# Performance work log

Measured on AMD Instinct MI355X. Metric: run time of the kernel, lower is better.

The kernel has to match this reference:

```python
import jax, jax.numpy as jnp
import numpy as np

NEG_INF = -9e15
ALPHA = 0.2  # leaky relu negative slope


def setup_inputs() -> dict:
    key = jax.random.key(0)
    ks = jax.random.split(key, 7)
    B, N, FIN, FOUT = 4, 2048, 512, 128
    inp = {
        "input": jax.random.normal(ks[0], (B, N, FIN), dtype=jnp.float32),
        "W": jax.random.normal(ks[1], (FIN, FOUT), dtype=jnp.float32) * (1.414 / np.sqrt(FIN)),
        "a1": jax.random.normal(ks[2], (FOUT, 1), dtype=jnp.float32) * 0.1,
        "a2": jax.random.normal(ks[3], (FOUT, 1), dtype=jnp.float32) * 0.1,
        "adj": jax.random.randint(ks[4], (B, N, N), 0, 4, dtype=jnp.int32),
        "adj_tree": jax.random.randint(ks[5], (B, N, N), 0, 4, dtype=jnp.int32),
        "d1": 1,
        "d2": 2,
    }
    return inp


def reference(input, W, a1, a2, adj, adj_tree, d1, d2):
    # adj_tree is accepted but unused by the original forward.
    h = jnp.einsum("bnf,fo->bno", input, W)          # [B,N,out]
    t1 = jnp.einsum("bno,ok->bnk", h, a1)            # [B,N,1]
    t2 = jnp.einsum("bno,ok->bnk", h, a2)            # [B,N,1]
    # e[b,i,j] = t1[b,i] + t2[b,j]  (broadcast add, no repeat needed)
    e = jax.nn.leaky_relu(t1 + jnp.swapaxes(t2, 1, 2), negative_slope=ALPHA)
    att = jnp.where(adj == d1, e, NEG_INF)
    att = jnp.where(adj == d2, e, att)
    att = jax.nn.softmax(att, axis=2)
    # dropout is identity in eval mode (training=False)
    h_prime = jnp.einsum("bij,bjo->bio", att, h)     # [B,N,out]
    return h_prime
```

## Files before the change

### kernel.cpp

```cpp
#include <hip/hip_runtime.h>
#include <hip/hip_bf16.h>

#define NN 2048
#define FIN 512
#define FOUT 128
#define NEGV -9e15f
#define ALPHAV 0.2f

typedef __attribute__((ext_vector_type(8))) short bf16x8;
typedef __attribute__((ext_vector_type(4))) float f32x4;

__device__ __forceinline__ unsigned cvt_pk_bf16(float lo, float hi) {
    unsigned r;
    asm("v_cvt_pk_bf16_f32 %0, %1, %2" : "=v"(r) : "v"(lo), "v"(hi));
    return r;
}

__device__ __forceinline__ unsigned short f32_to_bf16(float f) {
    unsigned int u = __float_as_uint(f);
    unsigned int r = (u + 0x7FFFu + ((u >> 16) & 1u)) >> 16;
    return (unsigned short)r;
}

__global__ void k_wrep(const float* __restrict__ W,
                       unsigned short* __restrict__ whi,
                       unsigned short* __restrict__ wlo) {
    int kt = blockIdx.x >> 3;
    int t_o = blockIdx.x & 7;
    int l = threadIdx.x;
    int lr = l & 15, lg = l >> 4;
    unsigned short vh[8], vl[8];
#pragma unroll
    for (int jj = 0; jj < 8; jj++) {
        float f = W[(size_t)(kt * 32 + lg * 8 + jj) * FOUT + t_o * 16 + lr];
        unsigned short h = f32_to_bf16(f);
        float hf = __uint_as_float(((unsigned)h) << 16);
        vh[jj] = h;
        vl[jj] = f32_to_bf16(f - hf);
    }
    size_t o = ((size_t)(kt * 8 + t_o) * 64 + l) * 8;
    *(uint4*)(whi + o) = *(const uint4*)vh;
    *(uint4*)(wlo + o) = *(const uint4*)vl;
}

__global__ void __launch_bounds__(256) k_h(const float* __restrict__ x,
                                           const unsigned short* __restrict__ whi,
                                           const unsigned short* __restrict__ wlo,
                                           const float* __restrict__ a1,
                                           const float* __restrict__ a2,
                                           unsigned short* __restrict__ hb,
                                           float* __restrict__ t1,
                                           float* __restrict__ t2) {
    __shared__ float lds_t1[4][16];
    __shared__ float lds_t2[4][16];
    int blk = blockIdx.x;
    int tid = threadIdx.x;
    int wv = tid >> 6, l = tid & 63;
    int lr = l & 15, lg = l >> 4;
    int row0 = blk * 16;

    const float* xp = x + (size_t)(row0 + lr) * FIN + lg * 8;
    const unsigned short* wb = whi + (size_t)(2 * wv) * 512 + l * 8;
    const unsigned short* lb = wlo + (size_t)(2 * wv) * 512 + l * 8;

    f32x4 acc0 = {0.f, 0.f, 0.f, 0.f};
    f32x4 acc1 = {0.f, 0.f, 0.f, 0.f};

#pragma unroll 2
    for (int kt = 0; kt < FIN / 32; kt++) {
        float4 xa = *(const float4*)(xp + kt * 32);
        float4 xb = *(const float4*)(xp + kt * 32 + 4);
        bf16x8 wh0 = *(const bf16x8*)(wb + (size_t)kt * 4096);
        bf16x8 wh1 = *(const bf16x8*)(wb + (size_t)kt * 4096 + 512);
        bf16x8 wl0 = *(const bf16x8*)(lb + (size_t)kt * 4096);
        bf16x8 wl1 = *(const bf16x8*)(lb + (size_t)kt * 4096 + 512);

        float f[8] = {xa.x, xa.y, xa.z, xa.w, xb.x, xb.y, xb.z, xb.w};
        unsigned uh[4], ul[4];
#pragma unroll
        for (int w = 0; w < 4; w++) {
            uh[w] = cvt_pk_bf16(f[2 * w], f[2 * w + 1]);
            float r0 = f[2 * w]     - __uint_as_float(uh[w] << 16);
            float r1 = f[2 * w + 1] - __uint_as_float(uh[w] & 0xffff0000u);
            ul[w] = cvt_pk_bf16(r0, r1);
        }
        bf16x8 xh = *(const bf16x8*)uh;
        bf16x8 xl = *(const bf16x8*)ul;

        acc0 = __builtin_amdgcn_mfma_f32_16x16x32_bf16(xh, wh0, acc0, 0, 0, 0);
        acc0 = __builtin_amdgcn_mfma_f32_16x16x32_bf16(xl, wh0, acc0, 0, 0, 0);
        acc0 = __builtin_amdgcn_mfma_f32_16x16x32_bf16(xh, wl0, acc0, 0, 0, 0);
        acc1 = __builtin_amdgcn_mfma_f32_16x16x32_bf16(xh, wh1, acc1, 0, 0, 0);
        acc1 = __builtin_amdgcn_mfma_f32_16x16x32_bf16(xl, wh1, acc1, 0, 0, 0);
        acc1 = __builtin_amdgcn_mfma_f32_16x16x32_bf16(xh, wl1, acc1, 0, 0, 0);
    }

    {
        float a10 = a1[(2 * wv) * 16 + lr], a11 = a1[(2 * wv + 1) * 16 + lr];
        float a20 = a2[(2 * wv) * 16 + lr], a21 = a2[(2 * wv + 1) * 16 + lr];
        float p1[4], p2[4];
#pragma unroll
        for (int r = 0; r < 4; r++) {
            p1[r] = acc0[r] * a10 + acc1[r] * a11;
            p2[r] = acc0[r] * a20 + acc1[r] * a21;
        }
#pragma unroll
        for (int off = 1; off < 16; off <<= 1) {
#pragma unroll
            for (int r = 0; r < 4; r++) {
                p1[r] += __shfl_xor(p1[r], off);
                p2[r] += __shfl_xor(p2[r], off);
            }
        }
        if (lr == 0) {
#pragma unroll
            for (int r = 0; r < 4; r++) {
                lds_t1[wv][lg * 4 + r] = p1[r];
                lds_t2[wv][lg * 4 + r] = p2[r];
            }
        }
        __syncthreads();
        if (tid < 16) {
            t1[row0 + tid] = lds_t1[0][tid] + lds_t1[1][tid] + lds_t1[2][tid] + lds_t1[3][tid];
            t2[row0 + tid] = lds_t2[0][tid] + lds_t2[1][tid] + lds_t2[2][tid] + lds_t2[3][tid];
        }
    }

    {
        size_t jtg = (size_t)(blk >> 1);
        int srcbase = (2 * (lg & 1)) * 16 + lr;
        bool active = (lg >> 1) == (blk & 1);
#pragma unroll
        for (int t = 0; t < 2; t++) {
            f32x4 a = t == 0 ? acc0 : acc1;
            unsigned p0 = cvt_pk_bf16(a[0], a[1]);
            unsigned p1 = cvt_pk_bf16(a[2], a[3]);
            unsigned g0 = __shfl((int)p0, srcbase);
            unsigned g1 = __shfl((int)p1, srcbase);
            unsigned g2 = __shfl((int)p0, srcbase + 16);
            unsigned g3 = __shfl((int)p1, srcbase + 16);
            if (active) {
                uint4 v = {g0, g1, g2, g3};
                int t_o = 2 * wv + t;
                *(uint4*)(hb + (jtg * 8 + t_o) * 512 + l * 8) = v;
            }
        }
    }
}

__global__ void __launch_bounds__(256) k_attn(const int* __restrict__ adj,
                                              const float* __restrict__ t1g,
                                              const float* __restrict__ t2g,
                                              const unsigned short* __restrict__ hb,
                                              const int* __restrict__ d1p,
                                              const int* __restrict__ d2p,
                                              float* __restrict__ out) {
    __shared__ float accbuf[4][16][132];
    __shared__ float lds_m[4][16];
    __shared__ float lds_s[4][16];
    __shared__ float lds_inv[16];

    int blk = blockIdx.x;
    int b = blk >> 7;
    int i0 = (blk & 127) * 16;
    int tid = threadIdx.x;
    int wv = tid >> 6;
    int l = tid & 63;
    int lr = l & 15, lg = l >> 4;
    int d1 = d1p[0], d2 = d2p[0];

    float t1v = t1g[b * NN + i0 + lr];
    const int* adjRow = adj + ((size_t)(b * NN + i0 + lr)) * NN + lg * 8;
    const float* t2p = t2g + b * NN + lg * 8;
    const unsigned short* hbbase = hb + (size_t)b * 64 * 4096 + (size_t)l * 8;

    float m = NEGV, s = 0.f;
    f32x4 acc[8];
#pragma unroll
    for (int t = 0; t < 8; t++) acc[t] = (f32x4){0.f, 0.f, 0.f, 0.f};

#pragma unroll 2
    for (int jt = wv; jt < NN / 32; jt += 4) {
        int4 av0 = *(const int4*)(adjRow + jt * 32);
        int4 av1 = *(const int4*)(adjRow + jt * 32 + 4);
        float4 tb0 = *(const float4*)(t2p + jt * 32);
        float4 tb1 = *(const float4*)(t2p + jt * 32 + 4);
        bf16x8 hf[8];
#pragma unroll
        for (int t = 0; t < 8; t++)
            hf[t] = *(const bf16x8*)(hbbase + (size_t)jt * 4096 + t * 512);

        int ai[8] = {av0.x, av0.y, av0.z, av0.w, av1.x, av1.y, av1.z, av1.w};
        float tv[8] = {tb0.x, tb0.y, tb0.z, tb0.w, tb1.x, tb1.y, tb1.z, tb1.w};
        float att[8];
#pragma unroll
        for (int jj = 0; jj < 8; jj++) {
            float v = t1v + tv[jj];
            float e = fmaxf(v, ALPHAV * v);
            att[jj] = (ai[jj] == d1 || ai[jj] == d2) ? e : NEGV;
        }
        float mx = att[0];
#pragma unroll
        for (int jj = 1; jj < 8; jj++) mx = fmaxf(mx, att[jj]);
        mx = fmaxf(mx, __shfl_xor(mx, 16));
        mx = fmaxf(mx, __shfl_xor(mx, 32));

        if (__any(mx > m + 8.f)) {
            float mnew = fmaxf(m, mx);
            float scale = __expf(m - mnew);
            m = mnew;
            s *= scale;
            float scr[4];
#pragma unroll
            for (int r = 0; r < 4; r++) scr[r] = __shfl(scale, lg * 4 + r);
#pragma unroll
            for (int t = 0; t < 8; t++)
#pragma unroll
                for (int r = 0; r < 4; r++) acc[t][r] *= scr[r];
        }

        float p[8];
        float psum = 0.f;
#pragma unroll
        for (int jj = 0; jj < 8; jj++) {
            p[jj] = __expf(att[jj] - m);
            psum += p[jj];
        }
        s += psum;

        unsigned u[4];
#pragma unroll
        for (int w = 0; w < 4; w++) u[w] = cvt_pk_bf16(p[2 * w], p[2 * w + 1]);
        bf16x8 pa = *(const bf16x8*)u;
#pragma unroll
        for (int t = 0; t < 8; t++)
            acc[t] = __builtin_amdgcn_mfma_f32_16x16x32_bf16(pa, hf[t], acc[t], 0, 0, 0);
    }

    s += __shfl_xor(s, 16);
    s += __shfl_xor(s, 32);
    if (l < 16) { lds_m[wv][lr] = m; lds_s[wv][lr] = s; }
    __syncthreads();

    float mt = fmaxf(fmaxf(lds_m[0][lr], lds_m[1][lr]),
                     fmaxf(lds_m[2][lr], lds_m[3][lr]));
    if (wv == 0 && l < 16) {
        float st = 0.f;
#pragma unroll
        for (int w = 0; w < 4; w++) st += lds_s[w][lr] * __expf(lds_m[w][lr] - mt);
        lds_inv[lr] = 1.0f / st;
    }
    float scale = __expf(m - mt);
    float scr[4];
#pragma unroll
    for (int r = 0; r < 4; r++) scr[r] = __shfl(scale, lg * 4 + r);
#pragma unroll
    for (int t = 0; t < 8; t++)
#pragma unroll
        for (int r = 0; r < 4; r++)
            accbuf[wv][lg * 4 + r][t * 16 + lr] = acc[t][r] * scr[r];
    __syncthreads();

#pragma unroll
    for (int e = 0; e < 8; e++) {
        int flat = tid + e * 256;
        int row = flat >> 7;
        int col = flat & 127;
        float sum = accbuf[0][row][col] + accbuf[1][row][col]
                  + accbuf[2][row][col] + accbuf[3][row][col];
        out[((size_t)b * NN + i0 + row) * FOUT + col] = sum * lds_inv[row];
    }
}

extern "C" void kernel_launch(void* const* d_in, const int* in_sizes, int n_in,
                              void* d_out, int out_size, void* d_ws, size_t ws_size,
                              hipStream_t stream) {
    const float* x  = (const float*)d_in[0];
    const float* W  = (const float*)d_in[1];
    const float* a1 = (const float*)d_in[2];
    const float* a2 = (const float*)d_in[3];
    const int* adj  = (const int*)d_in[4];
    const int* d1p  = (const int*)d_in[6];
    const int* d2p  = (const int*)d_in[7];
    float* out = (float*)d_out;

    char* ws = (char*)d_ws;
    unsigned short* hbuf = (unsigned short*)(ws);
    float* t1            = (float*)(ws + 2u * 1024 * 1024);
    float* t2            = (float*)(ws + 2u * 1024 * 1024 + 32 * 1024);
    unsigned short* whi  = (unsigned short*)(ws + 2u * 1024 * 1024 + 64 * 1024);
    unsigned short* wlo  = (unsigned short*)(ws + 2u * 1024 * 1024 + 192 * 1024);

    k_wrep<<<dim3(128), dim3(64), 0, stream>>>(W, whi, wlo);
    k_h<<<dim3(512), dim3(256), 0, stream>>>(x, whi, wlo, a1, a2, hbuf, t1, t2);
    k_attn<<<dim3(512), dim3(256), 0, stream>>>(adj, t1, t2, hbuf, d1p, d2p, out);
}
```

Measured before the change: 44.60 us.

## Drop online softmax max tracking, use exp2 with prescaled logits, 8 waves per block

```diff
diff --git a/kernel.cpp b/kernel.cpp
--- a/kernel.cpp
+++ b/kernel.cpp
@@ -6,6 +6,7 @@
 #define FOUT 128
 #define NEGV -9e15f
 #define ALPHAV 0.2f
+#define LOG2E 1.44269504088896340736f
 
 typedef __attribute__((ext_vector_type(8))) short bf16x8;
 typedef __attribute__((ext_vector_type(4))) float f32x4;
@@ -121,8 +122,8 @@
         }
         __syncthreads();
         if (tid < 16) {
-            t1[row0 + tid] = lds_t1[0][tid] + lds_t1[1][tid] + lds_t1[2][tid] + lds_t1[3][tid];
-            t2[row0 + tid] = lds_t2[0][tid] + lds_t2[1][tid] + lds_t2[2][tid] + lds_t2[3][tid];
+            t1[row0 + tid] = (lds_t1[0][tid] + lds_t1[1][tid] + lds_t1[2][tid] + lds_t1[3][tid]) * LOG2E;
+            t2[row0 + tid] = (lds_t2[0][tid] + lds_t2[1][tid] + lds_t2[2][tid] + lds_t2[3][tid]) * LOG2E;
         }
     }
 
@@ -148,16 +149,15 @@
     }
 }
 
-__global__ void __launch_bounds__(256) k_attn(const int* __restrict__ adj,
-                                              const float* __restrict__ t1g,
-                                              const float* __restrict__ t2g,
-                                              const unsigned short* __restrict__ hb,
-                                              const int* __restrict__ d1p,
-                                              const int* __restrict__ d2p,
-                                              float* __restrict__ out) {
-    __shared__ float accbuf[4][16][132];
-    __shared__ float lds_m[4][16];
-    __shared__ float lds_s[4][16];
+__global__ void __launch_bounds__(512, 4) k_attn(const int* __restrict__ adj,
+                                                 const float* __restrict__ t1g,
+                                                 const float* __restrict__ t2g,
+                                                 const unsigned short* __restrict__ hb,
+                                                 const int* __restrict__ d1p,
+                                                 const int* __restrict__ d2p,
+                                                 float* __restrict__ out) {
+    __shared__ __align__(16) float accbuf[4][16][132];
+    __shared__ float lds_s[8][16];
     __shared__ float lds_inv[16];
 
     int blk = blockIdx.x;
@@ -174,13 +174,13 @@
     const float* t2p = t2g + b * NN + lg * 8;
     const unsigned short* hbbase = hb + (size_t)b * 64 * 4096 + (size_t)l * 8;
 
-    float m = NEGV, s = 0.f;
+    float s = 0.f;
     f32x4 acc[8];
 #pragma unroll
     for (int t = 0; t < 8; t++) acc[t] = (f32x4){0.f, 0.f, 0.f, 0.f};
 
 #pragma unroll 2
-    for (int jt = wv; jt < NN / 32; jt += 4) {
+    for (int jt = wv; jt < NN / 32; jt += 8) {
         int4 av0 = *(const int4*)(adjRow + jt * 32);
         int4 av1 = *(const int4*)(adjRow + jt * 32 + 4);
         float4 tb0 = *(const float4*)(t2p + jt * 32);
@@ -192,38 +192,14 @@
 
         int ai[8] = {av0.x, av0.y, av0.z, av0.w, av1.x, av1.y, av1.z, av1.w};
         float tv[8] = {tb0.x, tb0.y, tb0.z, tb0.w, tb1.x, tb1.y, tb1.z, tb1.w};
-        float att[8];
+        float p[8];
+        float psum = 0.f;
 #pragma unroll
         for (int jj = 0; jj < 8; jj++) {
             float v = t1v + tv[jj];
             float e = fmaxf(v, ALPHAV * v);
-            att[jj] = (ai[jj] == d1 || ai[jj] == d2) ? e : NEGV;
-        }
-        float mx = att[0];
-#pragma unroll
-        for (int jj = 1; jj < 8; jj++) mx = fmaxf(mx, att[jj]);
-        mx = fmaxf(mx, __shfl_xor(mx, 16));
-        mx = fmaxf(mx, __shfl_xor(mx, 32));
-
-        if (__any(mx > m + 8.f)) {
-            float mnew = fmaxf(m, mx);
-            float scale = __expf(m - mnew);
-            m = mnew;
-            s *= scale;
-            float scr[4];
-#pragma unroll
-            for (int r = 0; r < 4; r++) scr[r] = __shfl(scale, lg * 4 + r);
-#pragma unroll
-            for (int t = 0; t < 8; t++)
-#pragma unroll
-                for (int r = 0; r < 4; r++) acc[t][r] *= scr[r];
-        }
-
-        float p[8];
-        float psum = 0.f;
-#pragma unroll
-        for (int jj = 0; jj < 8; jj++) {
-            p[jj] = __expf(att[jj] - m);
+            float att = (ai[jj] == d1 || ai[jj] == d2) ? e : NEGV;
+            p[jj] = __builtin_amdgcn_exp2f(att);
             psum += p[jj];
         }
         s += psum;
@@ -239,36 +215,45 @@
 
     s += __shfl_xor(s, 16);
     s += __shfl_xor(s, 32);
-    if (l < 16) { lds_m[wv][lr] = m; lds_s[wv][lr] = s; }
+    if (l < 16) lds_s[wv][lr] = s;
+
+    if (wv < 4) {
+#pragma unroll
+        for (int t = 0; t < 8; t++)
+#pragma unroll
+            for (int r = 0; r < 4; r++)
+                accbuf[wv][lg * 4 + r][t * 16 + lr] = acc[t][r];
+    }
     __syncthreads();
-
-    float mt = fmaxf(fmaxf(lds_m[0][lr], lds_m[1][lr]),
-                     fmaxf(lds_m[2][lr], lds_m[3][lr]));
-    if (wv == 0 && l < 16) {
+    if (wv >= 4) {
+#pragma unroll
+        for (int t = 0; t < 8; t++)
+#pragma unroll
+            for (int r = 0; r < 4; r++)
+                accbuf[wv - 4][lg * 4 + r][t * 16 + lr] += acc[t][r];
+    }
+    if (tid < 16) {
         float st = 0.f;
 #pragma unroll
-        for (int w = 0; w < 4; w++) st += lds_s[w][lr] * __expf(lds_m[w][lr] - mt);
-        lds_inv[lr] = 1.0f / st;
-    }
-    float scale = __expf(m - mt);
-    float scr[4];
-#pragma unroll
-    for (int r = 0; r < 4; r++) scr[r] = __shfl(scale, lg * 4 + r);
-#pragma unroll
-    for (int t = 0; t < 8; t++)
-#pragma unroll
-        for (int r = 0; r < 4; r++)
-            accbuf[wv][lg * 4 + r][t * 16 + lr] = acc[t][r] * scr[r];
+        for (int w = 0; w < 8; w++) st += lds_s[w][tid];
+        lds_inv[tid] = 1.0f / st;
+    }
     __syncthreads();
 
-#pragma unroll
-    for (int e = 0; e < 8; e++) {
-        int flat = tid + e * 256;
-        int row = flat >> 7;
-        int col = flat & 127;
-        float sum = accbuf[0][row][col] + accbuf[1][row][col]
-                  + accbuf[2][row][col] + accbuf[3][row][col];
-        out[((size_t)b * NN + i0 + row) * FOUT + col] = sum * lds_inv[row];
+    {
+        int row = tid >> 5;
+        int c4 = (tid & 31) * 4;
+        float4 s0 = *(const float4*)&accbuf[0][row][c4];
+        float4 s1 = *(const float4*)&accbuf[1][row][c4];
+        float4 s2 = *(const float4*)&accbuf[2][row][c4];
+        float4 s3 = *(const float4*)&accbuf[3][row][c4];
+        float inv = lds_inv[row];
+        float4 o;
+        o.x = (s0.x + s1.x + s2.x + s3.x) * inv;
+        o.y = (s0.y + s1.y + s2.y + s3.y) * inv;
+        o.z = (s0.z + s1.z + s2.z + s3.z) * inv;
+        o.w = (s0.w + s1.w + s2.w + s3.w) * inv;
+        *(float4*)&out[((size_t)b * NN + i0 + row) * FOUT + c4] = o;
     }
 }
 
@@ -293,5 +278,5 @@
 
     k_wrep<<<dim3(128), dim3(64), 0, stream>>>(W, whi, wlo);
     k_h<<<dim3(512), dim3(256), 0, stream>>>(x, whi, wlo, a1, a2, hbuf, t1, t2);
-    k_attn<<<dim3(512), dim3(256), 0, stream>>>(adj, t1, t2, hbuf, d1p, d2p, out);
-}
+    k_attn<<<dim3(512), dim3(512), 0, stream>>>(adj, t1, t2, hbuf, d1p, d2p, out);
+}
```

Measured after the change: 47.27 us. 6.0% more time.
